# Kernel optimization log

Hardware: AMD Instinct MI355X
Metric: run time of the kernel (lower is better)

The kernel has to match this reference:

```python
import jax, jax.numpy as jnp
import numpy as np

EPS = 1e-5


def setup_inputs() -> dict:
    key = jax.random.key(0)
    ks = jax.random.split(key, 5)
    B, C, H, W = 64, 512, 28, 28
    G = 8
    c_half = C // (2 * G)  # 32
    return {
        "x": jax.random.normal(ks[0], (B, C, H, W), dtype=jnp.float32),
        "cweight": jax.random.normal(ks[1], (c_half,), dtype=jnp.float32),
        "cbias": jax.random.normal(ks[2], (c_half,), dtype=jnp.float32),
        "sweight": jax.random.normal(ks[3], (c_half,), dtype=jnp.float32),
        "sbias": jax.random.normal(ks[4], (c_half,), dtype=jnp.float32),
        "G": G,
    }


def reference(x, cweight, cbias, sweight, sbias, G):
    B, C, H, W = x.shape
    HW = H * W
    Cg = C // G
    c_half = Cg // 2

    # group view: [B*G, Cg, HW]
    xg = x.reshape(B * G, Cg, HW)
    x0 = xg[:, :c_half]   # channel-attention half
    x1 = xg[:, c_half:]   # spatial-attention half

    # channel attention: sigmoid(cweight * avgpool_hw(x0) + cbias), per channel
    m = jnp.mean(x0, axis=-1, keepdims=True)                    # [BG, c_half, 1]
    a0 = jax.nn.sigmoid(cweight[None, :, None] * m + cbias[None, :, None])
    y0 = x0 * a0

    # spatial attention: GN stats over the whole c_half*HW slab per (b,g)
    mu = jnp.mean(x1, axis=(1, 2), keepdims=True)               # [BG, 1, 1]
    var = jnp.mean(x1 * x1, axis=(1, 2), keepdims=True) - mu * mu
    rstd = jax.lax.rsqrt(jnp.maximum(var, 0.0) + EPS)
    norm = (x1 - mu) * rstd
    a1 = jax.nn.sigmoid(sweight[None, :, None] * norm + sbias[None, :, None])
    y1 = x1 * a1

    y = jnp.concatenate([y0, y1], axis=1).reshape(B, C, HW)

    # channel shuffle with 2 groups: out[:, 2*w + g2] = y[:, g2*(C//2) + w]
    y = y.reshape(B, 2, C // 2, HW).transpose(0, 2, 1, 3).reshape(B, C, H, W)
    return y
```

## Files before the change

kernel.cpp:

```cpp
#include <hip/hip_runtime.h>

typedef float f32x4 __attribute__((ext_vector_type(4)));

#define EPSV 1e-5f

__device__ __forceinline__ float sigmoidf_(float z) {
    return 1.0f / (1.0f + __expf(-z));
}

__global__ __launch_bounds__(512, 8) void fused_sgate_mix(
    const f32x4* __restrict__ x4,
    const float* __restrict__ cweight,
    const float* __restrict__ cbias,
    const float* __restrict__ sweight,
    const float* __restrict__ sbias,
    f32x4* __restrict__ out4)
{
    const int bid = (int)blockIdx.x;
    const int tid = threadIdx.x;

    if (bid % 5 == 0) {
        const int bg = bid / 5;
        const int b  = bg >> 3, g = bg & 7;
        const f32x4* __restrict__ xs = x4 + (size_t)bg * 12544 + 6272;

        float s = 0.f, ss = 0.f;
#pragma unroll
        for (int k = 0; k < 12; ++k) {
            f32x4 v = xs[tid + 512 * k];
            s  += (v.x + v.y) + (v.z + v.w);
            ss += (v.x * v.x + v.y * v.y) + (v.z * v.z + v.w * v.w);
        }
        const bool x1e = (tid < 128);
        if (x1e) {
            f32x4 v = xs[6144 + tid];
            s  += (v.x + v.y) + (v.z + v.w);
            ss += (v.x * v.x + v.y * v.y) + (v.z * v.z + v.w * v.w);
        }

#pragma unroll
        for (int m = 32; m >= 1; m >>= 1) {
            s  += __shfl_xor(s,  m, 64);
            ss += __shfl_xor(ss, m, 64);
        }

        __shared__ float lds_s[8], lds_ss[8];
        __shared__ float ldsA[32], ldsB[32];
        if ((tid & 63) == 0) { lds_s[tid >> 6] = s; lds_ss[tid >> 6] = ss; }
        __syncthreads();

        if (tid < 32) {
            float S = 0.f, SS = 0.f;
#pragma unroll
            for (int i = 0; i < 8; ++i) { S += lds_s[i]; SS += lds_ss[i]; }
            constexpr float inv_n = 1.0f / (32.0f * 784.0f);
            const float mu   = S * inv_n;
            const float var  = SS * inv_n - mu * mu;
            const float rstd = rsqrtf(fmaxf(var, 0.f) + EPSV);
            const float A    = sweight[tid] * rstd;
            ldsA[tid] = A;
            ldsB[tid] = sbias[tid] - A * mu;
        }
        __syncthreads();

        f32x4* __restrict__ ob = out4 + (size_t)b * 100352;
#pragma unroll
        for (int k = 0; k < 12; ++k) {
            const int idx = tid + 512 * k;
            const int c1  = idx / 196;
            const int p   = idx - c1 * 196;
            const float A = ldsA[c1], Bq = ldsB[c1];
            f32x4 t = xs[idx], r;
            r.x = t.x * sigmoidf_(A * t.x + Bq);
            r.y = t.y * sigmoidf_(A * t.y + Bq);
            r.z = t.z * sigmoidf_(A * t.z + Bq);
            r.w = t.w * sigmoidf_(A * t.w + Bq);
            const int c  = g * 64 + 32 + c1;
            const int cp = (c < 256) ? (2 * c) : (2 * (c - 256) + 1);
            __builtin_nontemporal_store(r, ob + (size_t)cp * 196 + p);
        }
        if (x1e) {
            const int idx = 6144 + tid;
            const int c1  = idx / 196;
            const int p   = idx - c1 * 196;
            const float A = ldsA[c1], Bq = ldsB[c1];
            f32x4 t = xs[idx], r;
            r.x = t.x * sigmoidf_(A * t.x + Bq);
            r.y = t.y * sigmoidf_(A * t.y + Bq);
            r.z = t.z * sigmoidf_(A * t.z + Bq);
            r.w = t.w * sigmoidf_(A * t.w + Bq);
            const int c  = g * 64 + 32 + c1;
            const int cp = (c < 256) ? (2 * c) : (2 * (c - 256) + 1);
            __builtin_nontemporal_store(r, ob + (size_t)cp * 196 + p);
        }
    } else {
        const int x0id = bid - bid / 5 - 1;
        const int chw  = x0id * 8 + (tid >> 6);
        const int ln   = tid & 63;
        const int bg   = chw >> 5;
        const int cc   = chw & 31;

        const f32x4* __restrict__ xch = x4 + (size_t)bg * 12544 + cc * 196;
        f32x4 v0 = xch[ln];
        f32x4 v1 = xch[64 + ln];
        f32x4 v2 = xch[128 + ln];
        const bool extra = (ln < 4);
        f32x4 v3 = {0.f, 0.f, 0.f, 0.f};
        if (extra) v3 = xch[192 + ln];

        float s = (v0.x + v0.y) + (v0.z + v0.w)
                + (v1.x + v1.y) + (v1.z + v1.w)
                + (v2.x + v2.y) + (v2.z + v2.w)
                + (v3.x + v3.y) + (v3.z + v3.w);
#pragma unroll
        for (int m = 32; m >= 1; m >>= 1) s += __shfl_xor(s, m, 64);

        const float a0 = sigmoidf_(cweight[cc] * (s * (1.0f / 784.0f)) + cbias[cc]);

        const int b = bg >> 3, g = bg & 7;
        const int c  = g * 64 + cc;
        const int cp = (c < 256) ? (2 * c) : (2 * (c - 256) + 1);
        f32x4* __restrict__ och = out4 + (size_t)b * 100352 + (size_t)cp * 196;

        __builtin_nontemporal_store(v0 * a0, &och[ln]);
        __builtin_nontemporal_store(v1 * a0, &och[64 + ln]);
        __builtin_nontemporal_store(v2 * a0, &och[128 + ln]);
        if (extra) __builtin_nontemporal_store(v3 * a0, &och[192 + ln]);
    }
}

extern "C" void kernel_launch(void* const* d_in, const int* in_sizes, int n_in,
                              void* d_out, int out_size, void* d_ws, size_t ws_size,
                              hipStream_t stream) {
    const float* x  = (const float*)d_in[0];
    const float* cw = (const float*)d_in[1];
    const float* cb = (const float*)d_in[2];
    const float* sw = (const float*)d_in[3];
    const float* sb = (const float*)d_in[4];
    float* out = (float*)d_out;

    const int B   = in_sizes[0] / (512 * 784);
    const int nX1 = B * 8;
    const int nX0 = B * 32;

    fused_sgate_mix<<<nX1 + nX0, 512, 0, stream>>>(
        (const f32x4*)x, cw, cb, sw, sb, (f32x4*)out);
}
```

Measured before the change: 219.5 us.

## Split into stats kernel and contiguous-output apply kernel with workspace

Replaces the single fused kernel with two kernels. The first computes per-channel sigmoid gates and the spatial GroupNorm affine coefficients for every (batch, group) and writes them to a workspace. The second streams x again and writes each block's contiguous slice of the channel-shuffled output, gathering from the two source groups that interleave into it. The goal is fully sequential output writes and even work per block, at the cost of reading x a second time, an extra launch, and dropping the nontemporal stores.

```diff
diff --git a/kernel.cpp b/kernel.cpp
--- a/kernel.cpp
+++ b/kernel.cpp
@@ -8,124 +8,151 @@
     return 1.0f / (1.0f + __expf(-z));
 }
 
-__global__ __launch_bounds__(512, 8) void fused_sgate_mix(
+__global__ __launch_bounds__(1024, 2) void stats_all(
     const f32x4* __restrict__ x4,
     const float* __restrict__ cweight,
     const float* __restrict__ cbias,
     const float* __restrict__ sweight,
     const float* __restrict__ sbias,
-    f32x4* __restrict__ out4)
+    float* __restrict__ ws)
 {
-    const int bid = (int)blockIdx.x;
+    const int bg  = blockIdx.x;
     const int tid = threadIdx.x;
+    const int w   = tid >> 6;
+    const int ln  = tid & 63;
+    const f32x4* __restrict__ xg = x4 + (size_t)bg * 12544;
 
-    if (bid % 5 == 0) {
-        const int bg = bid / 5;
-        const int b  = bg >> 3, g = bg & 7;
-        const f32x4* __restrict__ xs = x4 + (size_t)bg * 12544 + 6272;
+    __shared__ float lds_s[8], lds_ss[8];
 
+    if (w < 8) {
+        const int ch  = 4 * w + (ln >> 4);
+        const int l16 = ln & 15;
+        const f32x4* __restrict__ xc = xg + ch * 196;
+        float s = 0.f;
+#pragma unroll
+        for (int k = 0; k < 12; ++k) {
+            f32x4 v = xc[l16 + 16 * k];
+            s += (v.x + v.y) + (v.z + v.w);
+        }
+        if (l16 < 4) {
+            f32x4 v = xc[192 + l16];
+            s += (v.x + v.y) + (v.z + v.w);
+        }
+        s += __shfl_xor(s, 1, 64); s += __shfl_xor(s, 2, 64);
+        s += __shfl_xor(s, 4, 64); s += __shfl_xor(s, 8, 64);
+        if (l16 == 0) {
+            ws[(size_t)bg * 96 + ch] =
+                sigmoidf_(cweight[ch] * (s * (1.0f / 784.0f)) + cbias[ch]);
+        }
+    } else {
+        const f32x4* __restrict__ xs = xg + 6272 + (w - 8) * 784;
         float s = 0.f, ss = 0.f;
 #pragma unroll
         for (int k = 0; k < 12; ++k) {
-            f32x4 v = xs[tid + 512 * k];
+            f32x4 v = xs[ln + 64 * k];
             s  += (v.x + v.y) + (v.z + v.w);
             ss += (v.x * v.x + v.y * v.y) + (v.z * v.z + v.w * v.w);
         }
-        const bool x1e = (tid < 128);
-        if (x1e) {
-            f32x4 v = xs[6144 + tid];
+        if (ln < 16) {
+            f32x4 v = xs[768 + ln];
             s  += (v.x + v.y) + (v.z + v.w);
             ss += (v.x * v.x + v.y * v.y) + (v.z * v.z + v.w * v.w);
         }
-
 #pragma unroll
         for (int m = 32; m >= 1; m >>= 1) {
             s  += __shfl_xor(s,  m, 64);
             ss += __shfl_xor(ss, m, 64);
         }
+        if (ln == 0) { lds_s[w - 8] = s; lds_ss[w - 8] = ss; }
+    }
+    __syncthreads();
 
-        __shared__ float lds_s[8], lds_ss[8];
-        __shared__ float ldsA[32], ldsB[32];
-        if ((tid & 63) == 0) { lds_s[tid >> 6] = s; lds_ss[tid >> 6] = ss; }
-        __syncthreads();
+    if (tid < 32) {
+        float S = 0.f, SS = 0.f;
+#pragma unroll
+        for (int i = 0; i < 8; ++i) { S += lds_s[i]; SS += lds_ss[i]; }
+        constexpr float inv_n = 1.0f / (32.0f * 784.0f);
+        const float mu   = S * inv_n;
+        const float var  = SS * inv_n - mu * mu;
+        const float rstd = rsqrtf(fmaxf(var, 0.f) + EPSV);
+        const float A    = sweight[tid] * rstd;
+        ws[(size_t)bg * 96 + 32 + 2 * tid] = A;
+        ws[(size_t)bg * 96 + 33 + 2 * tid] = sbias[tid] - A * mu;
+    }
+}
 
-        if (tid < 32) {
-            float S = 0.f, SS = 0.f;
-#pragma unroll
-            for (int i = 0; i < 8; ++i) { S += lds_s[i]; SS += lds_ss[i]; }
-            constexpr float inv_n = 1.0f / (32.0f * 784.0f);
-            const float mu   = S * inv_n;
-            const float var  = SS * inv_n - mu * mu;
-            const float rstd = rsqrtf(fmaxf(var, 0.f) + EPSV);
-            const float A    = sweight[tid] * rstd;
-            ldsA[tid] = A;
-            ldsB[tid] = sbias[tid] - A * mu;
+__global__ __launch_bounds__(1024, 2) void apply_stream(
+    const f32x4* __restrict__ x4,
+    const float* __restrict__ ws,
+    f32x4* __restrict__ out4)
+{
+    const int bid = (int)blockIdx.x;
+    const int b   = bid >> 3;
+    const int gp  = (bid >> 1) & 3;
+    const int h   = bid & 1;
+    const int tid = threadIdx.x;
+
+    __shared__ float gA[64], gB[64];
+    if (tid < 64) {
+        const size_t src_bg = (size_t)(b * 8 + gp + 4 * (tid & 1));
+        if (h == 0) {
+            gA[tid] = ws[src_bg * 96 + (tid >> 1)];
+        } else {
+            gA[tid] = ws[src_bg * 96 + 32 + 2 * (tid >> 1)];
+            gB[tid] = ws[src_bg * 96 + 33 + 2 * (tid >> 1)];
         }
-        __syncthreads();
+    }
+    __syncthreads();
 
-        f32x4* __restrict__ ob = out4 + (size_t)b * 100352;
+    const size_t in_e = (size_t)(b * 8 + gp)     * 12544 + (size_t)h * 6272;
+    const size_t in_o = (size_t)(b * 8 + gp + 4) * 12544 + (size_t)h * 6272;
+    f32x4* __restrict__ ob =
+        out4 + (size_t)b * 100352 + (size_t)(gp * 128 + 64 * h) * 196;
+
+    if (h == 0) {
 #pragma unroll
         for (int k = 0; k < 12; ++k) {
-            const int idx = tid + 512 * k;
-            const int c1  = idx / 196;
-            const int p   = idx - c1 * 196;
-            const float A = ldsA[c1], Bq = ldsB[c1];
-            f32x4 t = xs[idx], r;
-            r.x = t.x * sigmoidf_(A * t.x + Bq);
-            r.y = t.y * sigmoidf_(A * t.y + Bq);
-            r.z = t.z * sigmoidf_(A * t.z + Bq);
-            r.w = t.w * sigmoidf_(A * t.w + Bq);
-            const int c  = g * 64 + 32 + c1;
-            const int cp = (c < 256) ? (2 * c) : (2 * (c - 256) + 1);
-            __builtin_nontemporal_store(r, ob + (size_t)cp * 196 + p);
+            const int idx = tid + 1024 * k;
+            const int r   = idx / 196;
+            const int p   = idx - r * 196;
+            const f32x4 v = x4[((r & 1) ? in_o : in_e) + (r >> 1) * 196 + p];
+            ob[idx] = v * gA[r];
         }
-        if (x1e) {
-            const int idx = 6144 + tid;
-            const int c1  = idx / 196;
-            const int p   = idx - c1 * 196;
-            const float A = ldsA[c1], Bq = ldsB[c1];
-            f32x4 t = xs[idx], r;
-            r.x = t.x * sigmoidf_(A * t.x + Bq);
-            r.y = t.y * sigmoidf_(A * t.y + Bq);
-            r.z = t.z * sigmoidf_(A * t.z + Bq);
-            r.w = t.w * sigmoidf_(A * t.w + Bq);
-            const int c  = g * 64 + 32 + c1;
-            const int cp = (c < 256) ? (2 * c) : (2 * (c - 256) + 1);
-            __builtin_nontemporal_store(r, ob + (size_t)cp * 196 + p);
+        if (tid < 256) {
+            const int idx = 12288 + tid;
+            const int r   = idx / 196;
+            const int p   = idx - r * 196;
+            const f32x4 v = x4[((r & 1) ? in_o : in_e) + (r >> 1) * 196 + p];
+            ob[idx] = v * gA[r];
         }
     } else {
-        const int x0id = bid - bid / 5 - 1;
-        const int chw  = x0id * 8 + (tid >> 6);
-        const int ln   = tid & 63;
-        const int bg   = chw >> 5;
-        const int cc   = chw & 31;
-
-        const f32x4* __restrict__ xch = x4 + (size_t)bg * 12544 + cc * 196;
-        f32x4 v0 = xch[ln];
-        f32x4 v1 = xch[64 + ln];
-        f32x4 v2 = xch[128 + ln];
-        const bool extra = (ln < 4);
-        f32x4 v3 = {0.f, 0.f, 0.f, 0.f};
-        if (extra) v3 = xch[192 + ln];
-
-        float s = (v0.x + v0.y) + (v0.z + v0.w)
-                + (v1.x + v1.y) + (v1.z + v1.w)
-                + (v2.x + v2.y) + (v2.z + v2.w)
-                + (v3.x + v3.y) + (v3.z + v3.w);
 #pragma unroll
-        for (int m = 32; m >= 1; m >>= 1) s += __shfl_xor(s, m, 64);
-
-        const float a0 = sigmoidf_(cweight[cc] * (s * (1.0f / 784.0f)) + cbias[cc]);
-
-        const int b = bg >> 3, g = bg & 7;
-        const int c  = g * 64 + cc;
-        const int cp = (c < 256) ? (2 * c) : (2 * (c - 256) + 1);
-        f32x4* __restrict__ och = out4 + (size_t)b * 100352 + (size_t)cp * 196;
-
-        __builtin_nontemporal_store(v0 * a0, &och[ln]);
-        __builtin_nontemporal_store(v1 * a0, &och[64 + ln]);
-        __builtin_nontemporal_store(v2 * a0, &och[128 + ln]);
-        if (extra) __builtin_nontemporal_store(v3 * a0, &och[192 + ln]);
+        for (int k = 0; k < 12; ++k) {
+            const int idx = tid + 1024 * k;
+            const int r   = idx / 196;
+            const int p   = idx - r * 196;
+            const f32x4 v = x4[((r & 1) ? in_o : in_e) + (r >> 1) * 196 + p];
+            const float A = gA[r], Bq = gB[r];
+            f32x4 rr;
+            rr.x = v.x * sigmoidf_(A * v.x + Bq);
+            rr.y = v.y * sigmoidf_(A * v.y + Bq);
+            rr.z = v.z * sigmoidf_(A * v.z + Bq);
+            rr.w = v.w * sigmoidf_(A * v.w + Bq);
+            ob[idx] = rr;
+        }
+        if (tid < 256) {
+            const int idx = 12288 + tid;
+            const int r   = idx / 196;
+            const int p   = idx - r * 196;
+            const f32x4 v = x4[((r & 1) ? in_o : in_e) + (r >> 1) * 196 + p];
+            const float A = gA[r], Bq = gB[r];
+            f32x4 rr;
+            rr.x = v.x * sigmoidf_(A * v.x + Bq);
+            rr.y = v.y * sigmoidf_(A * v.y + Bq);
+            rr.z = v.z * sigmoidf_(A * v.z + Bq);
+            rr.w = v.w * sigmoidf_(A * v.w + Bq);
+            ob[idx] = rr;
+        }
     }
 }
 
@@ -138,11 +165,13 @@
     const float* sw = (const float*)d_in[3];
     const float* sb = (const float*)d_in[4];
     float* out = (float*)d_out;
+    float* ws  = (float*)d_ws;
 
-    const int B   = in_sizes[0] / (512 * 784);
-    const int nX1 = B * 8;
-    const int nX0 = B * 32;
+    const int B = in_sizes[0] / (512 * 784);
 
-    fused_sgate_mix<<<nX1 + nX0, 512, 0, stream>>>(
-        (const f32x4*)x, cw, cb, sw, sb, (f32x4*)out);
+    stats_all<<<B * 8, 1024, 0, stream>>>(
+        (const f32x4*)x, cw, cb, sw, sb, ws);
+
+    apply_stream<<<B * 8, 1024, 0, stream>>>(
+        (const f32x4*)x, ws, (f32x4*)out);
 }
```

After: 204.1 us. 1.08x faster.
